# Optimization experiments

Measured on AMD Instinct MI355X. Metric: run time of the kernel, lower is better.

## Reference

```python
import jax, jax.numpy as jnp
import numpy as np

D_MODEL = 2048
D_INNER = 2048          # expand=1
N_HEADS = 32            # n_qk_heads == n_v_heads
D_STATE = 64
HEADDIM = D_INNER // N_HEADS  # 64
D_CONV = 4
CHUNK = 128
D_FF = 8192
EPS = 1e-5
CONV_DIM = D_INNER + 2 * N_HEADS * D_STATE            # 6144
D_IN_PROJ = 2 * D_INNER + 2 * N_HEADS * D_STATE + N_HEADS  # 8224


def rmsnorm(x, w, eps=EPS):
    x32 = x.astype(jnp.float32)
    x32 = x32 * jax.lax.rsqrt(jnp.mean(x32 * x32, axis=-1, keepdims=True) + eps)
    return (w * x32).astype(x.dtype)


def causal_conv1d(x, w, b):
    # x: (B, L, C), w: (C, K) depthwise, b: (C,). Causal left padding (K-1).
    K = w.shape[1]
    y = jax.lax.conv_general_dilated(
        x, jnp.transpose(w)[:, None, :],  # (K, 1, C)
        window_strides=(1,), padding=[(K - 1, 0)],
        dimension_numbers=("NWC", "WIO", "NWC"),
        feature_group_count=x.shape[-1])
    return y + b


def ssd_scan(x, dt, Bm, Cm, chunk=CHUNK):
    # Discrete Mamba2 SSD: h_t = exp(-softplus(dt_t)) * h_{t-1} + B_t (x) x_t; y_t = C_t . h_t
    # x: (b,l,h,p), dt: (b,l,h), Bm/Cm: (b,l,h,n)
    b, l, h, p = x.shape
    n = Bm.shape[-1]
    c = l // chunk
    xr = x.reshape(b, c, chunk, h, p)
    a_log = (-jax.nn.softplus(dt)).reshape(b, c, chunk, h)  # per-step log decay
    Br = Bm.reshape(b, c, chunk, h, n)
    Cr = Cm.reshape(b, c, chunk, h, n)
    cum = jnp.cumsum(a_log, axis=2)  # inclusive cumulative log-decay within chunk (b,c,q,h)
    # intra-chunk: scores[i,j] = exp(cum_i - cum_j) * (C_i . B_j), causal j <= i
    seg = jnp.exp(cum[:, :, :, None, :] - cum[:, :, None, :, :])       # (b,c,i,j,h)
    cb = jnp.einsum("bcihn,bcjhn->bcijh", Cr, Br)
    mask = jnp.tril(jnp.ones((chunk, chunk), bool))
    scores = jnp.where(mask[None, None, :, :, None], seg * cb, 0.0)
    y_intra = jnp.einsum("bcijh,bcjhp->bcihp", scores, xr)
    # per-chunk end state contribution
    decay_to_end = jnp.exp(cum[:, :, -1:, :] - cum)                     # (b,c,q,h)
    S = jnp.einsum("bcqh,bcqhn,bcqhp->bchnp", decay_to_end, Br, xr)
    A_chunk = jnp.exp(cum[:, :, -1, :])                                  # (b,c,h)
    def step(hprev, inp):
        Ac, Sc = inp
        return Ac[..., None, None] * hprev + Sc, hprev
    h0 = jnp.zeros((b, h, n, p), x.dtype)
    _, Hprev = jax.lax.scan(step, h0, (jnp.moveaxis(A_chunk, 1, 0), jnp.moveaxis(S, 1, 0)))
    Hprev = jnp.moveaxis(Hprev, 0, 1)  # state at each chunk start (b,c,h,n,p)
    y_inter = jnp.einsum("bcqh,bcqhn,bchnp->bcqhp", jnp.exp(cum), Cr, Hprev)
    return (y_intra + y_inter).reshape(b, l, h, p)


def mixer(u, in_proj_w, z_bias, conv_w, conv_b, D, out_proj_w):
    b, l, _ = u.shape
    zxbcdt = u @ in_proj_w.T  # (b,l,8224)
    z = zxbcdt[..., :D_INNER]
    xBC = zxbcdt[..., D_INNER:D_INNER + CONV_DIM]
    dt = zxbcdt[..., D_INNER + CONV_DIM:]  # (b,l,H)
    xBC = causal_conv1d(xBC, conv_w, conv_b)  # activation = identity
    x = xBC[..., :D_INNER].reshape(b, l, N_HEADS, HEADDIM)
    Bm = xBC[..., D_INNER:D_INNER + N_HEADS * D_STATE].reshape(b, l, N_HEADS, D_STATE)
    Cm = xBC[..., D_INNER + N_HEADS * D_STATE:].reshape(b, l, N_HEADS, D_STATE)
    y = ssd_scan(x, dt, Bm, Cm)
    y = y + D[None, None, :, None] * x  # D skip
    y = y.reshape(b, l, D_INNER)
    return (y * jax.nn.silu(z + z_bias)) @ out_proj_w.T


def setup_inputs() -> dict:
    key = jax.random.key(0)
    ks = jax.random.split(key, 8)
    s = 0.02
    return {
        "hidden_states": jax.random.normal(ks[0], (2, 2048, D_MODEL), jnp.float32),
        "in_proj_w": jax.random.normal(ks[1], (D_IN_PROJ, D_MODEL), jnp.float32) * s,
        "z_bias": jnp.zeros((D_INNER,), jnp.float32),
        "conv_w": jax.random.normal(ks[2], (CONV_DIM, D_CONV), jnp.float32) * s,
        "conv_b": jnp.zeros((CONV_DIM,), jnp.float32),
        "D": jnp.ones((N_HEADS,), jnp.float32),
        "out_proj_w": jax.random.normal(ks[3], (D_MODEL, D_INNER), jnp.float32) * s,
        "norm1_w": jnp.ones((D_MODEL,), jnp.float32),
        "norm2_w": jnp.ones((D_MODEL,), jnp.float32),
        "gate_w": jax.random.normal(ks[4], (D_FF, D_MODEL), jnp.float32) * s,
        "up_w": jax.random.normal(ks[5], (D_FF, D_MODEL), jnp.float32) * s,
        "down_w": jax.random.normal(ks[6], (D_MODEL, D_FF), jnp.float32) * s,
    }


def reference(hidden_states, in_proj_w, z_bias, conv_w, conv_b, D, out_proj_w,
              norm1_w, norm2_w, gate_w, up_w, down_w):
    residual = hidden_states
    h = rmsnorm(hidden_states, norm1_w)
    h = mixer(h, in_proj_w, z_bias, conv_w, conv_b, D, out_proj_w) + residual
    residual = h
    h = rmsnorm(h, norm2_w)
    h = (jax.nn.silu(h @ gate_w.T) * (h @ up_w.T)) @ down_w.T  # LlamaMLP
    return residual + h
```

## Files before the change

### kernel.cpp

```cpp
#include <hip/hip_runtime.h>


typedef unsigned short u16;
typedef __bf16 bf16x8 __attribute__((ext_vector_type(8)));
typedef float f32x4 __attribute__((ext_vector_type(4)));

#define D_MODEL   2048
#define D_INNER   2048
#define NH        32
#define CONV_DIM  6144
#define D_IN_PROJ 8224
#define NPAD      8320
#define DFF       8192
#define BATCH     2
#define SEQ       2048
#define M_TOK     4096
#define NCHUNK    16
#define CHUNK     128

__device__ __forceinline__ u16 f2b(float f) {
  union { float f; unsigned int u; } v; v.f = f;
  unsigned int r = v.u + 0x7FFFu + ((v.u >> 16) & 1u);
  return (u16)(r >> 16);
}
__device__ __forceinline__ float b2f(u16 u) {
  union { unsigned int u; float f; } v; v.u = ((unsigned int)u) << 16; return v.f;
}

__device__ __forceinline__ void async16(const void* g, void* l) {
  __builtin_amdgcn_global_load_lds((const __attribute__((address_space(1))) void*)g,
                                   (__attribute__((address_space(3))) void*)l, 16, 0, 0);
}

template <int EPI, int TN>
__global__ void __launch_bounds__(256, 4) gemm_bt(
    const u16* __restrict__ A, const u16* __restrict__ W,
    float* Cf, u16* Cb, const float* auxf, const u16* auxb, float* Fdt,
    int K, int Nreal) {
  constexpr int MI = (TN == 128) ? 4 : 2;
  __shared__ __align__(16) u16 sA[128 * 32];
  __shared__ __align__(16) u16 sB[TN * 32];
  const int tid = threadIdx.x;
  const int grid_n = gridDim.x >> 5;
  const int span = grid_n << 3;
  const int pid = blockIdx.x;
  const int bm = ((pid / span) << 3) + ((pid % span) & 7);
  const int bn = (pid % span) >> 3;
  const int lane = tid & 63;
  const int wave = tid >> 6;
  const int wm = (TN == 128) ? (wave >> 1) * 64 : wave * 32;
  const int wn = (TN == 128) ? (wave & 1) * 64 : 0;

  const f32x4 zero4 = {0.f, 0.f, 0.f, 0.f};
  f32x4 acc[MI][4];
#pragma unroll
  for (int i = 0; i < MI; ++i)
#pragma unroll
    for (int j = 0; j < 4; ++j) acc[i][j] = zero4;

  const int r0 = tid >> 2;
  const int kk = (tid & 3) * 8;
  const u16* ga0 = A + (size_t)(bm * 128 + r0) * K + kk;
  const u16* ga1 = ga0 + (size_t)64 * K;
  const u16* gb0 = W + (size_t)(bn * TN + r0) * K + kk;
  const u16* gb1 = gb0 + (size_t)64 * K;
  u16* la0 = &sA[tid * 8]; u16* la1 = &sA[2048 + tid * 8];
  u16* lb0 = &sB[tid * 8]; u16* lb1 = (TN == 128) ? &sB[2048 + tid * 8] : nullptr;

  const int lr = lane & 15;
  const int lk = (lane >> 4) * 8;

  for (int k0 = 0; k0 < K; k0 += 32) {
    async16(ga0, la0); async16(ga1, la1);
    async16(gb0, lb0);
    if (TN == 128) async16(gb1, lb1);
    ga0 += 32; ga1 += 32; gb0 += 32;
    if (TN == 128) gb1 += 32;
    __syncthreads();
    bf16x8 af[MI], bfv[4];
#pragma unroll
    for (int mi = 0; mi < MI; ++mi)
      af[mi] = *(const bf16x8*)&sA[(wm + mi * 16 + lr) * 32 + lk];
#pragma unroll
    for (int ni = 0; ni < 4; ++ni)
      bfv[ni] = *(const bf16x8*)&sB[(wn + ni * 16 + lr) * 32 + lk];
#pragma unroll
    for (int mi = 0; mi < MI; ++mi)
#pragma unroll
      for (int ni = 0; ni < 4; ++ni)
        acc[mi][ni] = __builtin_amdgcn_mfma_f32_16x16x32_bf16(af[mi], bfv[ni], acc[mi][ni], 0, 0, 0);
    __syncthreads();
  }

  const int er = (lane >> 4) * 4;
  const int ec = lane & 15;
#pragma unroll
  for (int mi = 0; mi < MI; ++mi) {
#pragma unroll
    for (int r = 0; r < 4; ++r) {
      const int grow = bm * 128 + wm + mi * 16 + er + r;
#pragma unroll
      for (int ni = 0; ni < 4; ++ni) {
        const int gcol = bn * TN + wn + ni * 16 + ec;
        if (gcol < Nreal) {
          const size_t idx = (size_t)grow * Nreal + gcol;
          const float v = acc[mi][ni][r];
          if (EPI == 1) {
            Cf[idx] = v + auxf[idx];
          } else if (EPI == 2) {
            const float g = b2f(auxb[idx]);
            const float sg = 1.f / (1.f + __expf(-g));
            Cb[idx] = f2b(v * g * sg);
          } else if (EPI == 3) {
            Cb[idx] = f2b(v);
            if (gcol >= D_INNER + CONV_DIM) Fdt[(size_t)grow * NH + (gcol - (D_INNER + CONV_DIM))] = v;
          } else {
            Cb[idx] = f2b(v);
          }
        }
      }
    }
  }
}

__global__ void cvt_kernel(const float* __restrict__ s, u16* __restrict__ d, int n4) {
  const int i = blockIdx.x * 256 + threadIdx.x;
  if (i >= n4) return;
  const float4 v = ((const float4*)s)[i];
  ushort4 r;
  r.x = f2b(v.x); r.y = f2b(v.y); r.z = f2b(v.z); r.w = f2b(v.w);
  ((ushort4*)d)[i] = r;
}

__global__ void rmsnorm_kernel(const float* __restrict__ x, const float* __restrict__ w,
                               u16* __restrict__ o) {
  const int row = blockIdx.x;
  const float* xr = x + (size_t)row * D_MODEL;
  float ss = 0.f;
  for (int c = threadIdx.x; c < D_MODEL; c += 256) { const float v = xr[c]; ss += v * v; }
#pragma unroll
  for (int off = 32; off > 0; off >>= 1) ss += __shfl_down(ss, off, 64);
  __shared__ float red[4];
  if ((threadIdx.x & 63) == 0) red[threadIdx.x >> 6] = ss;
  __syncthreads();
  const float scale = rsqrtf((red[0] + red[1] + red[2] + red[3]) * (1.f / D_MODEL) + 1e-5f);
  u16* orow = o + (size_t)row * D_MODEL;
  for (int c = threadIdx.x; c < D_MODEL; c += 256) orow[c] = f2b(xr[c] * scale * w[c]);
}

__global__ void conv_kernel(const u16* __restrict__ zx, const float* __restrict__ cw,
                            const float* __restrict__ cb, u16* __restrict__ out) {
  const int idx = blockIdx.x * 256 + threadIdx.x;
  const int ch = idx % CONV_DIM;
  const int m = idx / CONV_DIM;
  const int l = m & (SEQ - 1);
  float accv = cb[ch];
#pragma unroll
  for (int k = 0; k < 4; ++k) {
    const int ls = l - 3 + k;
    if (ls >= 0) accv += cw[ch * 4 + k] * b2f(zx[(size_t)(m - 3 + k) * D_IN_PROJ + D_INNER + ch]);
  }
  out[idx] = f2b(accv);
}

__global__ void dtcum_kernel(const float* __restrict__ dtbuf, float* __restrict__ cum) {
  const int blk = blockIdx.x;
  const int h = blk & 31, cc = (blk >> 5) & 15, b = blk >> 9;
  const int i = threadIdx.x;
  const int m = b * SEQ + cc * CHUNK + i;
  const float dt = dtbuf[(size_t)m * NH + h];
  const float sp = (dt > 20.f) ? dt : log1pf(__expf(dt));
  __shared__ float s[128];
  s[i] = -sp;
  __syncthreads();
  for (int off = 1; off < 128; off <<= 1) {
    const float v = (i >= off) ? s[i - off] : 0.f;
    __syncthreads();
    s[i] += v;
    __syncthreads();
  }
  cum[(size_t)m * NH + h] = s[i];
}

__global__ void state_kernel(const u16* __restrict__ xbc, const float* __restrict__ cum,
                             float* __restrict__ S) {
  const int blk = blockIdx.x;
  const int h = blk & 31, cc = (blk >> 5) & 15, b = blk >> 9;
  const int m0 = b * SEQ + cc * CHUNK;
  const int tid = threadIdx.x;
  const int tp = tid & 63, tg = tid >> 6;
  const int n0 = tg * 16;
  const float cl = cum[(size_t)(m0 + 127) * NH + h];
  __shared__ float sBq[32][64], sxq[32][64], sd[32];
  float accv[16];
#pragma unroll
  for (int i = 0; i < 16; ++i) accv[i] = 0.f;
  for (int q0 = 0; q0 < 128; q0 += 32) {
    __syncthreads();
    for (int e = tid; e < 2048; e += 256) {
      const int q = e >> 6, col = e & 63;
      const size_t rowb = (size_t)(m0 + q0 + q) * CONV_DIM;
      sBq[q][col] = b2f(xbc[rowb + D_INNER + h * 64 + col]);
      sxq[q][col] = b2f(xbc[rowb + h * 64 + col]);
    }
    if (tid < 32) sd[tid] = __expf(cl - cum[(size_t)(m0 + q0 + tid) * NH + h]);
    __syncthreads();
    for (int q = 0; q < 32; ++q) {
      const float xv = sxq[q][tp] * sd[q];
#pragma unroll
      for (int i = 0; i < 16; ++i) accv[i] += sBq[q][n0 + i] * xv;
    }
  }
  float* Sp = S + (((size_t)(b * 16 + cc) * NH + h) * 64) * 64;
#pragma unroll
  for (int i = 0; i < 16; ++i) Sp[(size_t)(n0 + i) * 64 + tp] = accv[i];
}

__global__ void scan_kernel(const float* __restrict__ S, const float* __restrict__ cum,
                            float* __restrict__ H) {
  const int idx = blockIdx.x * 256 + threadIdx.x;
  const int p = idx & 63, n = (idx >> 6) & 63, h = (idx >> 12) & 31, b = idx >> 17;
  float hs = 0.f;
  for (int cc = 0; cc < NCHUNK; ++cc) {
    const size_t off = (((size_t)(b * 16 + cc) * NH + h) * 64 + n) * 64 + p;
    H[off] = hs;
    const float Ac = __expf(cum[(size_t)(b * SEQ + cc * CHUNK + 127) * NH + h]);
    hs = Ac * hs + S[off];
  }
}

#define SPITCH 136
#define CPITCH 72
__global__ void __launch_bounds__(256, 2) y_kernel(
    const u16* __restrict__ xbc, const float* __restrict__ cum,
    const float* __restrict__ H, const float* __restrict__ Dp,
    const u16* __restrict__ zx, const float* __restrict__ zb,
    u16* __restrict__ yo) {
  const int blk = blockIdx.x;
  const int h = blk & 31, cc = (blk >> 5) & 15, b = blk >> 9;
  const int m0 = b * SEQ + cc * CHUNK;
  const int tid = threadIdx.x;
  const int lane = tid & 63, wave = tid >> 6;

  __shared__ __align__(16) u16 sC[128 * CPITCH];
  __shared__ __align__(16) u16 sU[64 * SPITCH + 64 * CPITCH];
  __shared__ __align__(16) u16 sP[128 * SPITCH];
  __shared__ float sCum[128];
  u16* sB = sU;
  u16* sxT = sU;
  u16* sHT = sU + 64 * SPITCH;

  {
    const int i = tid >> 4, n4 = (tid & 15) * 4;
    for (int i0 = 0; i0 < 128; i0 += 16) {
      const size_t g = (size_t)(m0 + i0 + i) * CONV_DIM + h * 64 + n4;
      *(ushort4*)&sC[(i0 + i) * CPITCH + n4] = *(const ushort4*)&xbc[g + 2 * D_INNER];
      *(ushort4*)&sB[(i0 + i) * CPITCH + n4] = *(const ushort4*)&xbc[g + D_INNER];
    }
    if (tid < 128) sCum[tid] = cum[(size_t)(m0 + tid) * NH + h];
  }
  __syncthreads();

  const int lr = lane & 15;
  const int lk = (lane >> 4) * 8;
  const int er = (lane >> 4) * 4;
  const int ec = lane & 15;

  {
    const int R = (wave >> 1) * 64, Cq = (wave & 1) * 64;
    const f32x4 z4 = {0.f, 0.f, 0.f, 0.f};
    f32x4 acc[4][4];
#pragma unroll
    for (int i = 0; i < 4; ++i)
#pragma unroll
      for (int j = 0; j < 4; ++j) acc[i][j] = z4;
#pragma unroll
    for (int k0 = 0; k0 < 64; k0 += 32) {
      bf16x8 af[4], bfv[4];
#pragma unroll
      for (int mi = 0; mi < 4; ++mi)
        af[mi] = *(const bf16x8*)&sC[(R + mi * 16 + lr) * CPITCH + k0 + lk];
#pragma unroll
      for (int ni = 0; ni < 4; ++ni)
        bfv[ni] = *(const bf16x8*)&sB[(Cq + ni * 16 + lr) * CPITCH + k0 + lk];
#pragma unroll
      for (int mi = 0; mi < 4; ++mi)
#pragma unroll
        for (int ni = 0; ni < 4; ++ni)
          acc[mi][ni] = __builtin_amdgcn_mfma_f32_16x16x32_bf16(af[mi], bfv[ni], acc[mi][ni], 0, 0, 0);
    }
#pragma unroll
    for (int mi = 0; mi < 4; ++mi)
#pragma unroll
      for (int r = 0; r < 4; ++r) {
        const int row = R + mi * 16 + er + r;
#pragma unroll
        for (int ni = 0; ni < 4; ++ni) {
          const int col = Cq + ni * 16 + ec;
          const float pv = (row >= col) ? __expf(sCum[row] - sCum[col]) * acc[mi][ni][r] : 0.f;
          sP[row * SPITCH + col] = f2b(pv);
        }
      }
  }
  __syncthreads();

  {
    const int i = tid >> 1, n32 = (tid & 1) * 32;
    const float sc = __expf(sCum[i]);
    for (int n = n32; n < n32 + 32; ++n)
      sC[i * CPITCH + n] = f2b(b2f(sC[i * CPITCH + n]) * sc);
  }
  {
    const int j = tid >> 1, p32 = (tid & 1) * 32;
    const size_t g = (size_t)(m0 + j) * CONV_DIM + h * 64;
    for (int p = p32; p < p32 + 32; ++p)
      sxT[p * SPITCH + j] = xbc[g + p];
    const float* Hp = H + (((size_t)(b * 16 + cc) * NH + h) * 64) * 64;
    if (j < 64) {
      const int n = j;
      for (int p = p32; p < p32 + 32; ++p)
        sHT[p * CPITCH + n] = f2b(Hp[n * 64 + p]);
    }
  }
  __syncthreads();

  {
    const int R2 = wave * 32;
    const f32x4 z4 = {0.f, 0.f, 0.f, 0.f};
    f32x4 acc[2][4];
#pragma unroll
    for (int i = 0; i < 2; ++i)
#pragma unroll
      for (int j = 0; j < 4; ++j) acc[i][j] = z4;
#pragma unroll
    for (int k0 = 0; k0 < 128; k0 += 32) {
      bf16x8 af[2], bfv[4];
#pragma unroll
      for (int mi = 0; mi < 2; ++mi)
        af[mi] = *(const bf16x8*)&sP[(R2 + mi * 16 + lr) * SPITCH + k0 + lk];
#pragma unroll
      for (int ni = 0; ni < 4; ++ni)
        bfv[ni] = *(const bf16x8*)&sxT[(ni * 16 + lr) * SPITCH + k0 + lk];
#pragma unroll
      for (int mi = 0; mi < 2; ++mi)
#pragma unroll
        for (int ni = 0; ni < 4; ++ni)
          acc[mi][ni] = __builtin_amdgcn_mfma_f32_16x16x32_bf16(af[mi], bfv[ni], acc[mi][ni], 0, 0, 0);
    }
#pragma unroll
    for (int k0 = 0; k0 < 64; k0 += 32) {
      bf16x8 af[2], bfv[4];
#pragma unroll
      for (int mi = 0; mi < 2; ++mi)
        af[mi] = *(const bf16x8*)&sC[(R2 + mi * 16 + lr) * CPITCH + k0 + lk];
#pragma unroll
      for (int ni = 0; ni < 4; ++ni)
        bfv[ni] = *(const bf16x8*)&sHT[(ni * 16 + lr) * CPITCH + k0 + lk];
#pragma unroll
      for (int mi = 0; mi < 2; ++mi)
#pragma unroll
        for (int ni = 0; ni < 4; ++ni)
          acc[mi][ni] = __builtin_amdgcn_mfma_f32_16x16x32_bf16(af[mi], bfv[ni], acc[mi][ni], 0, 0, 0);
    }
    const float Dh = Dp[h];
#pragma unroll
    for (int mi = 0; mi < 2; ++mi)
#pragma unroll
      for (int r = 0; r < 4; ++r) {
        const int row = R2 + mi * 16 + er + r;
        const int m = m0 + row;
#pragma unroll
        for (int ni = 0; ni < 4; ++ni) {
          const int p = ni * 16 + ec;
          const int gc = h * 64 + p;
          const float xv = b2f(sxT[p * SPITCH + row]);
          const float z = b2f(zx[(size_t)m * D_IN_PROJ + gc]) + zb[gc];
          const float sg = 1.f / (1.f + __expf(-z));
          yo[(size_t)m * D_INNER + gc] = f2b((acc[mi][ni][r] + Dh * xv) * z * sg);
        }
      }
  }
}

extern "C" void kernel_launch(void* const* d_in, const int* in_sizes, int n_in,
                              void* d_out, int out_size, void* d_ws, size_t ws_size,
                              hipStream_t stream) {
  (void)in_sizes; (void)n_in; (void)out_size; (void)ws_size;
  const float* hidden = (const float*)d_in[0];
  const float* w_in   = (const float*)d_in[1];
  const float* z_bias = (const float*)d_in[2];
  const float* conv_w = (const float*)d_in[3];
  const float* conv_b = (const float*)d_in[4];
  const float* Dp     = (const float*)d_in[5];
  const float* w_out  = (const float*)d_in[6];
  const float* n1w    = (const float*)d_in[7];
  const float* n2w    = (const float*)d_in[8];
  const float* w_g    = (const float*)d_in[9];
  const float* w_u    = (const float*)d_in[10];
  const float* w_d    = (const float*)d_in[11];
  float* out = (float*)d_out;

  char* p = (char*)d_ws;
  auto take = [&](size_t bytes) { char* r = p; p += (bytes + 255) & ~(size_t)255; return r; };
  u16*   Bzx  = (u16*)take((size_t)M_TOK * D_IN_PROJ * 2);
  u16*   Bxbc = (u16*)take((size_t)M_TOK * CONV_DIM * 2);
  float* F_cum = (float*)take((size_t)M_TOK * NH * 4);
  float* F_S   = (float*)take((size_t)BATCH * NCHUNK * NH * 64 * 64 * 4);
  float* F_H   = (float*)take((size_t)BATCH * NCHUNK * NH * 64 * 64 * 4);
  u16*   B_h   = (u16*)take((size_t)M_TOK * D_MODEL * 2);
  float* F_dt  = (float*)take((size_t)M_TOK * NH * 4);
  u16*   W_buf = (u16*)take((size_t)NPAD * D_MODEL * 2);
  u16* B_y    = (u16*)F_S;
  u16* B_gate = Bzx;
  u16* B_gu   = Bxbc;
  float* F_res2 = out;

  const int c2 = (D_MODEL * D_INNER / 4 + 255) / 256;
  const int c8 = (DFF * D_MODEL / 4 + 255) / 256;

  cvt_kernel<<<(D_IN_PROJ * D_MODEL / 4 + 255) / 256, 256, 0, stream>>>(w_in, W_buf, D_IN_PROJ * D_MODEL / 4);
  rmsnorm_kernel<<<M_TOK, 256, 0, stream>>>(hidden, n1w, B_h);
  gemm_bt<3, 128><<<(NPAD / 128) * 32, 256, 0, stream>>>(B_h, W_buf, nullptr, Bzx, nullptr, nullptr, F_dt, D_MODEL, D_IN_PROJ);

  conv_kernel<<<M_TOK * CONV_DIM / 256, 256, 0, stream>>>(Bzx, conv_w, conv_b, Bxbc);
  dtcum_kernel<<<BATCH * NCHUNK * NH, 128, 0, stream>>>(F_dt, F_cum);
  state_kernel<<<BATCH * NCHUNK * NH, 256, 0, stream>>>(Bxbc, F_cum, F_S);
  scan_kernel<<<BATCH * NH * 64 * 64 / 256, 256, 0, stream>>>(F_S, F_cum, F_H);
  y_kernel<<<BATCH * NCHUNK * NH, 256, 0, stream>>>(Bxbc, F_cum, F_H, Dp, Bzx, z_bias, B_y);

  cvt_kernel<<<c2, 256, 0, stream>>>(w_out, W_buf, D_MODEL * D_INNER / 4);
  gemm_bt<1, 64><<<(D_MODEL / 64) * 32, 256, 0, stream>>>(B_y, W_buf, F_res2, nullptr, hidden, nullptr, nullptr, D_INNER, D_MODEL);

  rmsnorm_kernel<<<M_TOK, 256, 0, stream>>>(F_res2, n2w, B_h);
  cvt_kernel<<<c8, 256, 0, stream>>>(w_g, W_buf, DFF * D_MODEL / 4);
  gemm_bt<4, 128><<<(DFF / 128) * 32, 256, 0, stream>>>(B_h, W_buf, nullptr, B_gate, nullptr, nullptr, nullptr, D_MODEL, DFF);
  cvt_kernel<<<c8, 256, 0, stream>>>(w_u, W_buf, DFF * D_MODEL / 4);
  gemm_bt<2, 128><<<(DFF / 128) * 32, 256, 0, stream>>>(B_h, W_buf, nullptr, B_gu, nullptr, B_gate, nullptr, D_MODEL, DFF);
  cvt_kernel<<<c8, 256, 0, stream>>>(w_d, W_buf, D_MODEL * DFF / 4);
  gemm_bt<1, 64><<<(D_MODEL / 64) * 32, 256, 0, stream>>>(B_gu, W_buf, out, nullptr, F_res2, nullptr, nullptr, DFF, D_MODEL);
}
```

Measured before the change: 1.358 ms.

## Replace GEMM with 256-wide, 4-stage pipelined kernel and fuse gate/up projection

Replaces the 128x128/128x64 single-buffered GEMM with a 512-thread kernel using 256-column tiles, a 4-slot LDS ring with prefetch two steps ahead, swizzled LDS addressing, XCD-aware workgroup remapping and raised MFMA priority. The gate and up weights are interleaved in 16-row groups into one matrix so a single GEMM computes both and applies SiLU*up in the epilogue. This removes the intermediate gate buffer and one weight conversion pass. The dt columns of in_proj are split into a separate small GEMM. Larger tiles cut global reloads and sync stalls but raise register and LDS pressure.

```diff
diff --git a/kernel.cpp b/kernel.cpp
--- a/kernel.cpp
+++ b/kernel.cpp
@@ -10,7 +10,6 @@
 #define NH        32
 #define CONV_DIM  6144
 #define D_IN_PROJ 8224
-#define NPAD      8320
 #define DFF       8192
 #define BATCH     2
 #define SEQ       2048
@@ -32,94 +31,160 @@
                                    (__attribute__((address_space(3))) void*)l, 16, 0, 0);
 }
 
-template <int EPI, int TN>
-__global__ void __launch_bounds__(256, 4) gemm_bt(
+template <int EPI, int BM>
+__global__ void __launch_bounds__(512, 2) gemm8(
     const u16* __restrict__ A, const u16* __restrict__ W,
-    float* Cf, u16* Cb, const float* auxf, const u16* auxb, float* Fdt,
-    int K, int Nreal) {
-  constexpr int MI = (TN == 128) ? 4 : 2;
-  __shared__ __align__(16) u16 sA[128 * 32];
-  __shared__ __align__(16) u16 sB[TN * 32];
+    float* Cf, u16* Cb, const float* __restrict__ auxf, float* Fdt,
+    int K, int Nbound, int ldC, int GN, int WR) {
+  constexpr int RB = BM / 32;
+  constexpr int CA = BM / 128;
+  constexpr int LPT = CA + 2;
+  constexpr int SLOT_A = BM * 32;
+  constexpr int SLOT_B = 256 * 32;
+  __shared__ __align__(16) u16 sA[4 * SLOT_A];
+  __shared__ __align__(16) u16 sB[4 * SLOT_B];
+
   const int tid = threadIdx.x;
-  const int grid_n = gridDim.x >> 5;
-  const int span = grid_n << 3;
-  const int pid = blockIdx.x;
-  const int bm = ((pid / span) << 3) + ((pid % span) & 7);
-  const int bn = (pid % span) >> 3;
-  const int lane = tid & 63;
-  const int wave = tid >> 6;
-  const int wm = (TN == 128) ? (wave >> 1) * 64 : wave * 32;
-  const int wn = (TN == 128) ? (wave & 1) * 64 : 0;
-
-  const f32x4 zero4 = {0.f, 0.f, 0.f, 0.f};
-  f32x4 acc[MI][4];
-#pragma unroll
-  for (int i = 0; i < MI; ++i)
-#pragma unroll
-    for (int j = 0; j < 4; ++j) acc[i][j] = zero4;
-
-  const int r0 = tid >> 2;
-  const int kk = (tid & 3) * 8;
-  const u16* ga0 = A + (size_t)(bm * 128 + r0) * K + kk;
-  const u16* ga1 = ga0 + (size_t)64 * K;
-  const u16* gb0 = W + (size_t)(bn * TN + r0) * K + kk;
-  const u16* gb1 = gb0 + (size_t)64 * K;
-  u16* la0 = &sA[tid * 8]; u16* la1 = &sA[2048 + tid * 8];
-  u16* lb0 = &sB[tid * 8]; u16* lb1 = (TN == 128) ? &sB[2048 + tid * 8] : nullptr;
+  const int lane = tid & 63, wave = tid >> 6;
+
+  const int nwg = gridDim.x;
+  const int q = nwg >> 3, r = nwg & 7, xc = blockIdx.x & 7, jj = blockIdx.x >> 3;
+  const int wg = (xc < r ? xc * (q + 1) : r * (q + 1) + (xc - r) * q) + jj;
+  const int bm = wg / GN, bn = wg % GN;
+
+  const int wrow = (wave >> 2) * (BM / 2);
+  const int wcol = (wave & 3) * 64;
+
+  const int l2 = lane >> 2;
+  const int cbl = (lane & 3) ^ ((lane >> 3) & 3);
+  const u16* pa[CA];
+  const u16* pb[2];
+#pragma unroll
+  for (int i = 0; i < CA; ++i)
+    pa[i] = A + (size_t)(bm * BM + (wave * CA + i) * 16 + l2) * K + cbl * 8;
+#pragma unroll
+  for (int i = 0; i < 2; ++i) {
+    int br = bn * 256 + (wave * 2 + i) * 16 + l2;
+    if (br >= WR) br = 0;
+    pb[i] = W + (size_t)br * K + cbl * 8;
+  }
+
+  auto stageA = [&](int slot) {
+#pragma unroll
+    for (int i = 0; i < CA; ++i) {
+      async16(pa[i], &sA[slot * SLOT_A + (wave * CA + i) * 512 + lane * 8]);
+      pa[i] += 32;
+    }
+  };
+  auto stageB = [&](int slot) {
+#pragma unroll
+    for (int i = 0; i < 2; ++i) {
+      async16(pb[i], &sB[slot * SLOT_B + (wave * 2 + i) * 512 + lane * 8]);
+      pb[i] += 32;
+    }
+  };
 
   const int lr = lane & 15;
-  const int lk = (lane >> 4) * 8;
-
-  for (int k0 = 0; k0 < K; k0 += 32) {
-    async16(ga0, la0); async16(ga1, la1);
-    async16(gb0, lb0);
-    if (TN == 128) async16(gb1, lb1);
-    ga0 += 32; ga1 += 32; gb0 += 32;
-    if (TN == 128) gb1 += 32;
-    __syncthreads();
-    bf16x8 af[MI], bfv[4];
-#pragma unroll
-    for (int mi = 0; mi < MI; ++mi)
-      af[mi] = *(const bf16x8*)&sA[(wm + mi * 16 + lr) * 32 + lk];
-#pragma unroll
-    for (int ni = 0; ni < 4; ++ni)
-      bfv[ni] = *(const bf16x8*)&sB[(wn + ni * 16 + lr) * 32 + lk];
-#pragma unroll
-    for (int mi = 0; mi < MI; ++mi)
-#pragma unroll
-      for (int ni = 0; ni < 4; ++ni)
-        acc[mi][ni] = __builtin_amdgcn_mfma_f32_16x16x32_bf16(af[mi], bfv[ni], acc[mi][ni], 0, 0, 0);
-    __syncthreads();
-  }
-
-  const int er = (lane >> 4) * 4;
-  const int ec = lane & 15;
-#pragma unroll
-  for (int mi = 0; mi < MI; ++mi) {
-#pragma unroll
-    for (int r = 0; r < 4; ++r) {
-      const int grow = bm * 128 + wm + mi * 16 + er + r;
-#pragma unroll
-      for (int ni = 0; ni < 4; ++ni) {
-        const int gcol = bn * TN + wn + ni * 16 + ec;
-        if (gcol < Nreal) {
-          const size_t idx = (size_t)grow * Nreal + gcol;
-          const float v = acc[mi][ni][r];
-          if (EPI == 1) {
-            Cf[idx] = v + auxf[idx];
-          } else if (EPI == 2) {
-            const float g = b2f(auxb[idx]);
-            const float sg = 1.f / (1.f + __expf(-g));
-            Cb[idx] = f2b(v * g * sg);
-          } else if (EPI == 3) {
-            Cb[idx] = f2b(v);
-            if (gcol >= D_INNER + CONV_DIM) Fdt[(size_t)grow * NH + (gcol - (D_INNER + CONV_DIM))] = v;
-          } else {
-            Cb[idx] = f2b(v);
+  const int afo = lr * 32 + ((((lane >> 4) ^ ((lr >> 1) & 3))) << 3);
+
+  f32x4 acc[RB][4];
+  const f32x4 z4 = {0.f, 0.f, 0.f, 0.f};
+#pragma unroll
+  for (int m = 0; m < RB; ++m)
+#pragma unroll
+    for (int n = 0; n < 4; ++n) acc[m][n] = z4;
+
+  const int NT = K >> 5;
+  stageA(0); stageB(0);
+  stageA(1); stageB(1);
+  asm volatile("s_waitcnt vmcnt(%0)" :: "n"(LPT) : "memory");
+  __builtin_amdgcn_s_barrier();
+  __builtin_amdgcn_sched_barrier(0);
+
+  for (int t = 0; t < NT; ++t) {
+    const int slot = t & 3;
+    const int s2 = (t + 2) & 3;
+    const bool pf = (t + 2 < NT);
+    const u16* sAs = &sA[slot * SLOT_A + wrow * 32 + afo];
+    const u16* sBs = &sB[slot * SLOT_B + wcol * 32 + afo];
+    bf16x8 av[4], bv[4];
+#pragma unroll
+    for (int m = 0; m < 4; ++m) av[m] = *(const bf16x8*)(sAs + m * 512);
+#pragma unroll
+    for (int n = 0; n < 4; ++n) bv[n] = *(const bf16x8*)(sBs + n * 512);
+    if (pf) stageA(s2);
+    if constexpr (RB == 4) { if (pf) stageB(s2); }
+    __builtin_amdgcn_s_barrier();
+    asm volatile("s_waitcnt lgkmcnt(0)" ::: "memory");
+    __builtin_amdgcn_sched_barrier(0);
+    __builtin_amdgcn_s_setprio(1);
+#pragma unroll
+    for (int m = 0; m < 4; ++m)
+#pragma unroll
+      for (int n = 0; n < 4; ++n)
+        acc[m][n] = __builtin_amdgcn_mfma_f32_16x16x32_bf16(av[m], bv[n], acc[m][n], 0, 0, 0);
+    __builtin_amdgcn_s_setprio(0);
+    if constexpr (RB == 8) {
+      __builtin_amdgcn_s_barrier();
+      __builtin_amdgcn_sched_barrier(0);
+#pragma unroll
+      for (int m = 0; m < 4; ++m) av[m] = *(const bf16x8*)(sAs + (m + 4) * 512);
+      if (pf) stageB(s2);
+      __builtin_amdgcn_s_barrier();
+      asm volatile("s_waitcnt lgkmcnt(0)" ::: "memory");
+      __builtin_amdgcn_sched_barrier(0);
+      __builtin_amdgcn_s_setprio(1);
+#pragma unroll
+      for (int m = 0; m < 4; ++m)
+#pragma unroll
+        for (int n = 0; n < 4; ++n)
+          acc[m + 4][n] = __builtin_amdgcn_mfma_f32_16x16x32_bf16(av[m], bv[n], acc[m + 4][n], 0, 0, 0);
+      __builtin_amdgcn_s_setprio(0);
+    }
+    if (pf) { asm volatile("s_waitcnt vmcnt(%0)" :: "n"(LPT) : "memory"); }
+    else    { asm volatile("s_waitcnt vmcnt(0)" ::: "memory"); }
+    __builtin_amdgcn_s_barrier();
+    __builtin_amdgcn_sched_barrier(0);
+  }
+
+  const int er = (lane >> 4) * 4, ec = lane & 15;
+  const int bmb = bm * BM + wrow, bnb = bn * 256 + wcol;
+  if constexpr (EPI == 6) {
+#pragma unroll
+    for (int m = 0; m < RB; ++m)
+#pragma unroll
+      for (int rr = 0; rr < 4; ++rr) {
+        const size_t grow = bmb + m * 16 + er + rr;
+#pragma unroll
+        for (int n = 0; n < 4; n += 2) {
+          const int oc = ((bnb + n * 16) >> 5) * 16 + ec;
+          const float g = acc[m][n][rr], u = acc[m][n + 1][rr];
+          const float sg = 1.f / (1.f + __expf(-g));
+          Cb[grow * DFF + oc] = f2b(u * g * sg);
+        }
+      }
+  } else {
+#pragma unroll
+    for (int m = 0; m < RB; ++m)
+#pragma unroll
+      for (int rr = 0; rr < 4; ++rr) {
+        const int grow = bmb + m * 16 + er + rr;
+#pragma unroll
+        for (int n = 0; n < 4; ++n) {
+          const int gcol = bnb + n * 16 + ec;
+          if (gcol < Nbound) {
+            const float v = acc[m][n][rr];
+            if constexpr (EPI == 1) {
+              const size_t idx = (size_t)grow * ldC + gcol;
+              Cf[idx] = v + auxf[idx];
+            } else if constexpr (EPI == 4) {
+              Cb[(size_t)grow * ldC + gcol] = f2b(v);
+            } else if constexpr (EPI == 5) {
+              Fdt[(size_t)grow * NH + gcol] = v;
+            }
           }
         }
       }
-    }
   }
 }
 
@@ -130,6 +195,21 @@
   ushort4 r;
   r.x = f2b(v.x); r.y = f2b(v.y); r.z = f2b(v.z); r.w = f2b(v.w);
   ((ushort4*)d)[i] = r;
+}
+
+__global__ void cvt_gateup_kernel(const float* __restrict__ g, const float* __restrict__ u,
+                                  u16* __restrict__ d) {
+  const int i = blockIdx.x * 256 + threadIdx.x;
+  const int total = 2 * DFF * D_MODEL / 4;
+  if (i >= total) return;
+  const int rowlen4 = D_MODEL / 4;
+  const int vrow = i / rowlen4, c4 = i % rowlen4;
+  const bool isg = vrow < DFF;
+  const int sr = isg ? vrow : vrow - DFF;
+  const float4 v = ((const float4*)(isg ? g : u))[(size_t)sr * rowlen4 + c4];
+  const int dr = (sr >> 4) * 32 + (isg ? 0 : 16) + (sr & 15);
+  ushort4 rr; rr.x = f2b(v.x); rr.y = f2b(v.y); rr.z = f2b(v.z); rr.w = f2b(v.w);
+  ((ushort4*)d)[(size_t)dr * rowlen4 + c4] = rr;
 }
 
 __global__ void rmsnorm_kernel(const float* __restrict__ x, const float* __restrict__ w,
@@ -409,18 +489,20 @@
   float* F_H   = (float*)take((size_t)BATCH * NCHUNK * NH * 64 * 64 * 4);
   u16*   B_h   = (u16*)take((size_t)M_TOK * D_MODEL * 2);
   float* F_dt  = (float*)take((size_t)M_TOK * NH * 4);
-  u16*   W_buf = (u16*)take((size_t)NPAD * D_MODEL * 2);
-  u16* B_y    = (u16*)F_S;
-  u16* B_gate = Bzx;
-  u16* B_gu   = Bxbc;
-  float* F_res2 = out;
+  u16*   W_buf = (u16*)take((size_t)D_IN_PROJ * D_MODEL * 2);
+  u16* B_y  = (u16*)F_S;
+  u16* W_gu = Bzx;
+  u16* B_gu = Bxbc;
 
   const int c2 = (D_MODEL * D_INNER / 4 + 255) / 256;
   const int c8 = (DFF * D_MODEL / 4 + 255) / 256;
 
   cvt_kernel<<<(D_IN_PROJ * D_MODEL / 4 + 255) / 256, 256, 0, stream>>>(w_in, W_buf, D_IN_PROJ * D_MODEL / 4);
   rmsnorm_kernel<<<M_TOK, 256, 0, stream>>>(hidden, n1w, B_h);
-  gemm_bt<3, 128><<<(NPAD / 128) * 32, 256, 0, stream>>>(B_h, W_buf, nullptr, Bzx, nullptr, nullptr, F_dt, D_MODEL, D_IN_PROJ);
+  gemm8<4, 256><<<16 * 32, 512, 0, stream>>>(B_h, W_buf, nullptr, Bzx, nullptr, nullptr,
+                                             D_MODEL, 8192, D_IN_PROJ, 32, 8192);
+  gemm8<5, 128><<<32, 512, 0, stream>>>(B_h, W_buf + (size_t)8192 * D_MODEL, nullptr, nullptr,
+                                        nullptr, F_dt, D_MODEL, NH, 0, 1, 32);
 
   conv_kernel<<<M_TOK * CONV_DIM / 256, 256, 0, stream>>>(Bzx, conv_w, conv_b, Bxbc);
   dtcum_kernel<<<BATCH * NCHUNK * NH, 128, 0, stream>>>(F_dt, F_cum);
@@ -429,13 +511,14 @@
   y_kernel<<<BATCH * NCHUNK * NH, 256, 0, stream>>>(Bxbc, F_cum, F_H, Dp, Bzx, z_bias, B_y);
 
   cvt_kernel<<<c2, 256, 0, stream>>>(w_out, W_buf, D_MODEL * D_INNER / 4);
-  gemm_bt<1, 64><<<(D_MODEL / 64) * 32, 256, 0, stream>>>(B_y, W_buf, F_res2, nullptr, hidden, nullptr, nullptr, D_INNER, D_MODEL);
-
-  rmsnorm_kernel<<<M_TOK, 256, 0, stream>>>(F_res2, n2w, B_h);
-  cvt_kernel<<<c8, 256, 0, stream>>>(w_g, W_buf, DFF * D_MODEL / 4);
-  gemm_bt<4, 128><<<(DFF / 128) * 32, 256, 0, stream>>>(B_h, W_buf, nullptr, B_gate, nullptr, nullptr, nullptr, D_MODEL, DFF);
-  cvt_kernel<<<c8, 256, 0, stream>>>(w_u, W_buf, DFF * D_MODEL / 4);
-  gemm_bt<2, 128><<<(DFF / 128) * 32, 256, 0, stream>>>(B_h, W_buf, nullptr, B_gu, nullptr, B_gate, nullptr, D_MODEL, DFF);
+  gemm8<1, 128><<<32 * 8, 512, 0, stream>>>(B_y, W_buf, out, nullptr, hidden, nullptr,
+                                            D_INNER, D_MODEL, D_MODEL, 8, 2048);
+
+  rmsnorm_kernel<<<M_TOK, 256, 0, stream>>>(out, n2w, B_h);
+  cvt_gateup_kernel<<<2 * DFF * D_MODEL / 4 / 256, 256, 0, stream>>>(w_g, w_u, W_gu);
+  gemm8<6, 256><<<16 * 64, 512, 0, stream>>>(B_h, W_gu, nullptr, B_gu, nullptr, nullptr,
+                                             D_MODEL, 2 * DFF, 0, 64, 16384);
   cvt_kernel<<<c8, 256, 0, stream>>>(w_d, W_buf, D_MODEL * DFF / 4);
-  gemm_bt<1, 64><<<(D_MODEL / 64) * 32, 256, 0, stream>>>(B_gu, W_buf, out, nullptr, F_res2, nullptr, nullptr, DFF, D_MODEL);
-}
+  gemm8<1, 128><<<32 * 8, 512, 0, stream>>>(B_gu, W_buf, out, nullptr, out,
+                                            nullptr, DFF, D_MODEL, D_MODEL, 8, 2048);
+}
```

New measurement: 1.165 ms. 1.17x faster.
